# Kernel tuning notes

Measured on AMD Instinct MI355X. Metric: run time of the kernel, lower is better.

## Reference

```python
import jax, jax.numpy as jnp
import numpy as np

N_NODES, N_GRAPHS, N_EDGES = 40960, 1024, 163840


def setup_inputs() -> dict:
    key = jax.random.key(0)
    ks = jax.random.split(key, 40)
    w = lambda k, s: jax.random.normal(k, s, jnp.float32) * 0.05
    inp = {
        "x": jax.random.normal(ks[0], (N_NODES, 78), jnp.float32),
        "edge_index": jax.random.randint(ks[1], (2, N_EDGES), 0, N_NODES, jnp.int32),
        "batch": jnp.repeat(jnp.arange(N_GRAPHS, dtype=jnp.int32), N_NODES // N_GRAPHS),
        "target1": jax.random.normal(ks[2], (N_GRAPHS, 750, 20), jnp.float32),
        "target2": jax.random.randint(ks[3], (N_GRAPHS, 750), 0, 26, jnp.int32),
        # GCN layers
        "W1": w(ks[4], (78, 78)), "b1": jnp.zeros((78,), jnp.float32),
        "W2": w(ks[5], (78, 156)), "b2": jnp.zeros((156,), jnp.float32),
        "W3": w(ks[6], (156, 312)), "b3": jnp.zeros((312,), jnp.float32),
        "Wg1": w(ks[7], (312, 1024)), "bg1": jnp.zeros((1024,), jnp.float32),
        "Wg2": w(ks[8], (1024, 128)), "bg2": jnp.zeros((128,), jnp.float32),
        # protein branch
        "emb": w(ks[9], (26, 128)),
        "Wc2": w(ks[10], (32, 750, 8)), "bc2": jnp.zeros((32,), jnp.float32),
        "Wxt2": w(ks[11], (32 * 121, 128)), "bxt2": jnp.zeros((128,), jnp.float32),
        "Wc1": w(ks[12], (32, 750, 8)), "bc1": jnp.zeros((32,), jnp.float32),
        "Wxt1": w(ks[13], (416, 128)), "bxt1": jnp.zeros((128,), jnp.float32),
        # fusion head
        "Wf1": w(ks[14], (384, 1024)), "bf1": jnp.zeros((1024,), jnp.float32),
        "Wf2": w(ks[15], (1024, 512)), "bf2": jnp.zeros((512,), jnp.float32),
        "Wo": w(ks[16], (512, 1)), "bo": jnp.zeros((1,), jnp.float32),
    }
    return inp


def _conv1d(x, w, b):
    # x: [B, C_in, L], w: [C_out, C_in, K] -> [B, C_out, L-K+1]
    y = jax.lax.conv_general_dilated(x, w, (1,), "VALID",
                                     dimension_numbers=("NCH", "OIH", "NCH"))
    return y + b[None, :, None]


def reference(x, edge_index, batch, target1, target2,
              W1, b1, W2, b2, W3, b3, Wg1, bg1, Wg2, bg2,
              emb, Wc2, bc2, Wxt2, bxt2, Wc1, bc1, Wxt1, bxt1,
              Wf1, bf1, Wf2, bf2, Wo, bo):
    N = x.shape[0]
    loop = jnp.arange(N, dtype=edge_index.dtype)
    src = jnp.concatenate([edge_index[0], loop])  # message source j
    dst = jnp.concatenate([edge_index[1], loop])  # aggregation target i
    # symmetric GCN normalization with self-loops (degree from dst, as in PyG)
    deg = jnp.zeros((N,), x.dtype).at[dst].add(1.0)
    dinv = jax.lax.rsqrt(deg)  # deg >= 1 due to self loops
    norm = (dinv[src] * dinv[dst])[:, None]

    def gcn(h, W, b):
        m = (h @ W)[src] * norm
        return jax.ops.segment_sum(m, dst, num_segments=N) + b

    h = jax.nn.relu(gcn(x, W1, b1))
    h = jax.nn.relu(gcn(h, W2, b2))
    h = jax.nn.relu(gcn(h, W3, b3))
    # global max pool per graph
    g = jax.ops.segment_max(h, batch, num_segments=N_GRAPHS)
    g = jax.nn.relu(g @ Wg1 + bg1)
    g = g @ Wg2 + bg2  # dropout is identity at inference

    # protein branch 2: embedding -> conv1d over channels=750
    e = emb[target2]                         # [B, 750, 128]
    xt2 = _conv1d(e, Wc2, bc2)               # [B, 32, 121]
    xt2 = xt2.reshape(-1, 32 * 121) @ Wxt2 + bxt2

    # protein branch 1: raw float features
    xt1 = _conv1d(target1, Wc1, bc1)         # [B, 32, 13]
    xt1 = xt1.reshape(-1, 416) @ Wxt1 + bxt1

    xc = jnp.concatenate([g, xt1, xt2], axis=1)  # [B, 384]
    xc = jax.nn.relu(xc @ Wf1 + bf1)
    xc = jax.nn.relu(xc @ Wf2 + bf2)
    return xc @ Wo + bo
```

## Files before the change

kernel.cpp:

```cpp
#include <hip/hip_runtime.h>
#include <hip/hip_bf16.h>

#define NN 40960
#define NE 163840
#define NB 1024

typedef __attribute__((ext_vector_type(8))) short short8;
typedef __attribute__((ext_vector_type(4))) short short4v;
typedef __attribute__((ext_vector_type(4))) float floatx4;

__device__ inline unsigned short f2bf(float f) {
    union { float f; unsigned u; } v; v.f = f;
    unsigned r = v.u + 0x7fffu + ((v.u >> 16) & 1u);
    return (unsigned short)(r >> 16);
}
__device__ inline float bf2f(unsigned short s) {
    union { unsigned u; float f; } v; v.u = ((unsigned)s) << 16; return v.f;
}
__device__ inline unsigned pack2bf(float lo, float hi) {
    return (unsigned)f2bf(lo) | ((unsigned)f2bf(hi) << 16);
}

static const size_t o_dinv = 0, o_g312 = 40960, o_g1024 = 360448, o_xc = 1409024,
                    o_f1 = 1802240, o_f2 = 2850816, o_b1v = 3375104, o_b2v = 3375232,
                    o_iws = 3375360, o_bufA = 3621124, o_bufB = 16400644;

__global__ void k_hist(const int* __restrict__ dst, int* __restrict__ cnt) {
    int e = blockIdx.x * 256 + threadIdx.x;
    if (e < NE) atomicAdd(&cnt[dst[e]], 1);
}

__global__ __launch_bounds__(1024) void k_scan1(const int* __restrict__ cnt, int* __restrict__ offTmp,
                                                int* __restrict__ blockSum, float* __restrict__ dinv) {
    __shared__ int lds[1024];
    int tid = threadIdx.x;
    int i = blockIdx.x * 1024 + tid;
    int v = cnt[i];
    dinv[i] = rsqrtf((float)v + 1.0f);
    lds[tid] = v;
    __syncthreads();
    for (int s = 1; s < 1024; s <<= 1) {
        int t = (tid >= s) ? lds[tid - s] : 0;
        __syncthreads();
        lds[tid] += t;
        __syncthreads();
    }
    offTmp[i] = lds[tid] - v;
    if (tid == 1023) blockSum[blockIdx.x] = lds[1023];
}

__global__ __launch_bounds__(64) void k_scan2(const int* __restrict__ blockSum, int* __restrict__ blockOff) {
    int l = threadIdx.x;
    int s = (l < 40) ? blockSum[l] : 0;
    int orig = s;
    for (int d = 1; d < 64; d <<= 1) {
        int t = __shfl_up(s, d);
        if (l >= d) s += t;
    }
    if (l < 40) blockOff[l] = s - orig;
}

__global__ __launch_bounds__(1024) void k_scan3(int* __restrict__ off, int* __restrict__ cur,
                                                const int* __restrict__ blockOff) {
    int i = blockIdx.x * 1024 + threadIdx.x;
    int o = off[i] + blockOff[blockIdx.x];
    off[i] = o;
    cur[i] = o;
    if (i == NN - 1) off[NN] = NE;
}

__global__ void k_fill(const int* __restrict__ ei, int* __restrict__ cur, int* __restrict__ srcOut) {
    int e = blockIdx.x * 256 + threadIdx.x;
    if (e >= NE) return;
    int s = ei[e], d = ei[NE + e];
    int pos = atomicAdd(&cur[d], 1);
    srcOut[pos] = s;
}

__global__ __launch_bounds__(256) void k_prep_mega(
    const float* __restrict__ W1, const float* __restrict__ W2, const float* __restrict__ W3,
    const float* __restrict__ Wg1, const float* __restrict__ Wg2, const float* __restrict__ Wf1,
    const float* __restrict__ Wf2, unsigned short* __restrict__ Wt,
    const float* __restrict__ Wc2, const float* __restrict__ Wc1,
    float* __restrict__ Wc2r, float* __restrict__ Wc1r,
    const float* __restrict__ Wxt1, float* __restrict__ Btb,
    const float* __restrict__ bc1, const float* __restrict__ bxt1, float* __restrict__ b1v,
    const float* __restrict__ bc2, const float* __restrict__ Wxt2, const float* __restrict__ bxt2,
    float* __restrict__ b2v,
    const float* __restrict__ emb, float* __restrict__ T) {
    __shared__ float el[128];
    int bx = blockIdx.x, tid = threadIdx.x;
    if (bx < 3328) {
        const int cum[8]  = {0, 128, 320, 640, 1664, 1792, 2816, 3328};
        const int KP[7]   = {96, 96, 160, 320, 1024, 384, 1024};
        const int KB[7]   = {78, 78, 156, 312, 1024, 384, 1024};
        const int NNm[7]  = {78, 156, 312, 1024, 128, 1024, 512};
        const size_t OFF[7] = {0, 12288, 30720, 81920, 409600, 540672, 933888};
        int m = 0;
        while (m < 6 && bx >= cum[m + 1]) m++;
        int r = bx - cum[m];
        const float* src = (m == 0) ? W1 : (m == 1) ? W2 : (m == 2) ? W3 : (m == 3) ? Wg1
                         : (m == 4) ? Wg2 : (m == 5) ? Wf1 : Wf2;
        int kp = KP[m], kb = KB[m], nn = NNm[m];
        unsigned short* d = Wt + OFF[m] + (size_t)r * kp;
        for (int k = tid; k < kp; k += 256) {
            float v = (r < nn && k < kb) ? src[(size_t)k * nn + r] : 0.f;
            d[k] = f2bf(v);
        }
    } else if (bx < 4828) {
        int cc = bx - 3328, j = tid;
        const float* W = (cc < 750) ? Wc2 : Wc1;
        float* Wr = (cc < 750) ? Wc2r : Wc1r;
        int c = (cc < 750) ? cc : cc - 750;
        Wr[(size_t)c * 256 + j] = W[(size_t)(j >> 3) * 6000 + c * 8 + (j & 7)];
    } else if (bx < 7388) {
        int idx = (bx - 4828) * 256 + tid;
        int j = idx & 127, ok = (idx >> 7) & 255, t = idx >> 15;
        int o = ok >> 3, k = ok & 7, lpos = t - k;
        float v = (lpos >= 0 && lpos < 13) ? Wxt1[(size_t)(o * 13 + lpos) * 128 + j] : 0.f;
        Btb[(size_t)(t * 256 + ok) * 128 + j] = v;
    } else if (bx < 7452) {
        if (tid >= 128) return;
        int b = bx - 7388, j = tid;
        if (b < 32) {
            const float* p = Wxt1 + (size_t)b * 13 * 128 + j;
            float t = 0.f;
            for (int l = 0; l < 13; l++) t += p[(size_t)l * 128];
            float add = bc1[b] * t + ((b == 0) ? bxt1[j] : 0.f);
            atomicAdd(&b1v[j], add);
        } else {
            int o = b - 32;
            const float* p = Wxt2 + (size_t)o * 121 * 128 + j;
            float t = 0.f;
            for (int l = 0; l < 121; l++) t += p[(size_t)l * 128];
            float add = bc2[o] * t + ((o == 0) ? bxt2[j] : 0.f);
            atomicAdd(&b2v[j], add);
        }
    } else {
        int tb = bx - 7452;
        int v = tb >> 4, op = tb & 15;
        int o = op * 2 + (tid >> 7), j = tid & 127;
        if (tid < 128) el[j] = emb[(size_t)v * 128 + j];
        __syncthreads();
        float acc[8] = {};
        for (int l = 0; l < 121; l++) {
            float w = Wxt2[(size_t)(o * 121 + l) * 128 + j];
#pragma unroll
            for (int k = 0; k < 8; k++) acc[k] += el[l + k] * w;
        }
#pragma unroll
        for (int k = 0; k < 8; k++) T[(size_t)(v * 256 + o * 8 + k) * 128 + j] = acc[k];
    }
}

__device__ inline void d_agg16_node(int n, int f, const unsigned* __restrict__ h,
                                    const float* __restrict__ dinv, const int* __restrict__ off,
                                    const int* __restrict__ srcs, unsigned* __restrict__ out, int F2) {
    if (f >= F2) return;
    float di = dinv[n];
    unsigned s0v = h[(size_t)n * F2 + f];
    float a0 = bf2f((unsigned short)(s0v & 0xffff)) * di * di;
    float a1 = bf2f((unsigned short)(s0v >> 16)) * di * di;
    int e0 = off[n], e1 = off[n + 1];
    int e = e0;
    for (; e + 4 <= e1; e += 4) {
        int s0 = srcs[e], s1 = srcs[e + 1], s2 = srcs[e + 2], s3 = srcs[e + 3];
        float d0 = dinv[s0] * di, d1 = dinv[s1] * di, d2 = dinv[s2] * di, d3 = dinv[s3] * di;
        unsigned v0 = h[(size_t)s0 * F2 + f];
        unsigned v1 = h[(size_t)s1 * F2 + f];
        unsigned v2 = h[(size_t)s2 * F2 + f];
        unsigned v3 = h[(size_t)s3 * F2 + f];
        a0 += bf2f((unsigned short)(v0 & 0xffff)) * d0 + bf2f((unsigned short)(v1 & 0xffff)) * d1
            + bf2f((unsigned short)(v2 & 0xffff)) * d2 + bf2f((unsigned short)(v3 & 0xffff)) * d3;
        a1 += bf2f((unsigned short)(v0 >> 16)) * d0 + bf2f((unsigned short)(v1 >> 16)) * d1
            + bf2f((unsigned short)(v2 >> 16)) * d2 + bf2f((unsigned short)(v3 >> 16)) * d3;
    }
    for (; e < e1; e++) {
        int s = srcs[e];
        float dd = dinv[s] * di;
        unsigned v = h[(size_t)s * F2 + f];
        a0 += bf2f((unsigned short)(v & 0xffff)) * dd;
        a1 += bf2f((unsigned short)(v >> 16)) * dd;
    }
    out[(size_t)n * F2 + f] = pack2bf(a0, a1);
}

__global__ void k_agg16(const unsigned* __restrict__ h, const float* __restrict__ dinv,
                        const int* __restrict__ off, const int* __restrict__ srcs,
                        unsigned* __restrict__ out, int F2) {
    d_agg16_node(blockIdx.x, threadIdx.x, h, dinv, off, srcs, out, F2);
}

#define LDST 72
template <bool ABF16, bool OUTBF16, bool ATOMIC, bool RELU_OUT>
__global__ __launch_bounds__(256) void gemm_bt(const void* __restrict__ Av, const unsigned short* __restrict__ Bt,
                                               const float* __restrict__ bias, void* __restrict__ Cv,
                                               int Nn, int Npad, int Kpad, int Klim,
                                               int lda, int ldb, int ldc, int ksplit) {
    __shared__ __align__(16) unsigned short As[64 * LDST];
    __shared__ __align__(16) unsigned short Bs[64 * LDST];
    const float* Af = (const float*)Av;
    const unsigned short* A16 = (const unsigned short*)Av;
    float* Cf = (float*)Cv;
    unsigned short* C16 = (unsigned short*)Cv;
    int bn0 = blockIdx.x * 64;
    int bm0 = blockIdx.y * 64;
    int k0 = blockIdx.z * ksplit;
    int kend = k0 + ksplit; if (kend > Kpad) kend = Kpad;
    int tid = threadIdx.x;
    int w = tid >> 6, l = tid & 63, q = l >> 4, r = l & 15;
    int wr = w >> 1, wc = w & 1;

    floatx4 acc[2][2];
#pragma unroll
    for (int i = 0; i < 2; i++)
#pragma unroll
        for (int c = 0; c < 2; c++) acc[i][c] = (floatx4)0.0f;

    int mA = tid >> 2, kcA = (tid & 3) * 8;
    int nB = tid >> 2, kcB = (tid & 3) * 8;
    int gmA = bm0 + mA;
    int gnB = bn0 + nB;

    for (int kt = k0; kt < kend; kt += 32) {
        if (ABF16) {
            *(short8*)&As[mA * LDST + kcA] = *(const short8*)(A16 + (size_t)gmA * lda + kt + kcA);
        } else {
            const float* Ap = Af + (size_t)gmA * lda + kt + kcA;
            float av[8];
            if (kt + kcA + 8 <= Klim) {
#pragma unroll
                for (int j = 0; j < 4; j++) {
                    float2 p = *(const float2*)(Ap + j * 2);
                    av[j * 2] = p.x; av[j * 2 + 1] = p.y;
                }
            } else {
#pragma unroll
                for (int j = 0; j < 8; j++) av[j] = (kt + kcA + j < Klim) ? Ap[j] : 0.f;
            }
            short8 sv;
#pragma unroll
            for (int j = 0; j < 8; j++) sv[j] = (short)f2bf(av[j]);
            *(short8*)&As[mA * LDST + kcA] = sv;
        }
        *(short8*)&Bs[nB * LDST + kcB] = *(const short8*)(Bt + (size_t)gnB * ldb + kt + kcB);
        __syncthreads();
        short8 a0 = *(const short8*)&As[(wr * 32 + r) * LDST + q * 8];
        short8 a1 = *(const short8*)&As[(wr * 32 + 16 + r) * LDST + q * 8];
        short8 b0 = *(const short8*)&Bs[(wc * 32 + r) * LDST + q * 8];
        short8 b1 = *(const short8*)&Bs[(wc * 32 + 16 + r) * LDST + q * 8];
        acc[0][0] = __builtin_amdgcn_mfma_f32_16x16x32_bf16(a0, b0, acc[0][0], 0, 0, 0);
        acc[0][1] = __builtin_amdgcn_mfma_f32_16x16x32_bf16(a0, b1, acc[0][1], 0, 0, 0);
        acc[1][0] = __builtin_amdgcn_mfma_f32_16x16x32_bf16(a1, b0, acc[1][0], 0, 0, 0);
        acc[1][1] = __builtin_amdgcn_mfma_f32_16x16x32_bf16(a1, b1, acc[1][1], 0, 0, 0);
        __syncthreads();
    }

#pragma unroll
    for (int c2 = 0; c2 < 2; c2++) {
        int col = bn0 + wc * 32 + c2 * 16 + r;
        if (col >= Npad) continue;
        bool live = col < Nn;
        float bv = (bias && live) ? bias[col] : 0.f;
#pragma unroll
        for (int i = 0; i < 2; i++) {
#pragma unroll
            for (int v = 0; v < 4; v++) {
                int row = bm0 + wr * 32 + i * 16 + q * 4 + v;
                float val = live ? (acc[i][c2][v] + bv) : 0.f;
                if (RELU_OUT) val = fmaxf(val, 0.f);
                if (OUTBF16) {
                    C16[(size_t)row * ldc + col] = live ? f2bf(val) : (unsigned short)0;
                } else if (live) {
                    if (ATOMIC) atomicAdd(&Cf[(size_t)row * ldc + col], val);
                    else Cf[(size_t)row * ldc + col] = val;
                }
            }
        }
    }
}

__global__ __launch_bounds__(256) void k_batch_both(const float* __restrict__ Wc2r, const float* __restrict__ T,
                                                    const float* __restrict__ Wc1r, const float* __restrict__ Btb,
                                                    unsigned short* __restrict__ U16, unsigned short* __restrict__ Vt16) {
    __shared__ __align__(16) unsigned short As[64 * LDST];
    __shared__ __align__(16) unsigned short Bs[64 * LDST];
    const int M = 750, Nn = 128, K = 256;
    int z = blockIdx.z;
    bool om1 = z < 26;
    const float* A = om1 ? Wc2r : Wc1r;
    const float* Bm = om1 ? (T + (size_t)z * 32768) : (Btb + (size_t)(z - 26) * 32768);
    unsigned short* C16 = om1 ? (U16 + (size_t)z * 128) : Vt16;
    int ldc = om1 ? 3328 : 15360;
    int zz = z - 26;
    int bn0 = blockIdx.x * 64;
    int bm0 = blockIdx.y * 64;
    int tid = threadIdx.x;
    int w = tid >> 6, l = tid & 63, q = l >> 4, r = l & 15;
    int wr = w >> 1, wc = w & 1;

    floatx4 acc[2][2];
#pragma unroll
    for (int i = 0; i < 2; i++)
#pragma unroll
        for (int c = 0; c < 2; c++) acc[i][c] = (floatx4)0.0f;

    int mA = tid >> 2, kcA = (tid & 3) * 8;
    int nB = tid >> 2, kcB = (tid & 3) * 8;
    int gmA = bm0 + mA;
    int gnB = bn0 + nB;

    for (int kt = 0; kt < K; kt += 32) {
        {
            float av[8];
            const float* Ap = A + (size_t)gmA * K + kt + kcA;
            if (gmA < M) {
#pragma unroll
                for (int j = 0; j < 4; j++) {
                    float2 p = *(const float2*)(Ap + j * 2);
                    av[j * 2] = p.x; av[j * 2 + 1] = p.y;
                }
            } else {
#pragma unroll
                for (int j = 0; j < 8; j++) av[j] = 0.f;
            }
            short8 sv;
#pragma unroll
            for (int j = 0; j < 8; j++) sv[j] = (short)f2bf(av[j]);
            *(short8*)&As[mA * LDST + kcA] = sv;
        }
        {
            short8 sv;
#pragma unroll
            for (int j = 0; j < 8; j++) {
                int gk = kt + kcB + j;
                float v = (gnB < Nn) ? Bm[(size_t)gk * Nn + gnB] : 0.f;
                sv[j] = (short)f2bf(v);
            }
            *(short8*)&Bs[nB * LDST + kcB] = sv;
        }
        __syncthreads();
        short8 a0 = *(const short8*)&As[(wr * 32 + r) * LDST + q * 8];
        short8 a1 = *(const short8*)&As[(wr * 32 + 16 + r) * LDST + q * 8];
        short8 b0 = *(const short8*)&Bs[(wc * 32 + r) * LDST + q * 8];
        short8 b1 = *(const short8*)&Bs[(wc * 32 + 16 + r) * LDST + q * 8];
        acc[0][0] = __builtin_amdgcn_mfma_f32_16x16x32_bf16(a0, b0, acc[0][0], 0, 0, 0);
        acc[0][1] = __builtin_amdgcn_mfma_f32_16x16x32_bf16(a0, b1, acc[0][1], 0, 0, 0);
        acc[1][0] = __builtin_amdgcn_mfma_f32_16x16x32_bf16(a1, b0, acc[1][0], 0, 0, 0);
        acc[1][1] = __builtin_amdgcn_mfma_f32_16x16x32_bf16(a1, b1, acc[1][1], 0, 0, 0);
        __syncthreads();
    }

#pragma unroll
    for (int c = 0; c < 2; c++) {
        int col = bn0 + wc * 32 + c * 16 + r;
        if (col >= Nn) continue;
#pragma unroll
        for (int i = 0; i < 2; i++) {
#pragma unroll
            for (int v = 0; v < 4; v++) {
                int row = bm0 + wr * 32 + i * 16 + q * 4 + v;
                if (row >= M) continue;
                if (om1) C16[(size_t)row * ldc + col] = f2bf(acc[i][c][v]);
                else C16[(size_t)col * ldc + row * 20 + zz] = f2bf(acc[i][c][v]);
            }
        }
    }
}

#define T1LD 40
#define T1S  48
#define T1K  320
__global__ __launch_bounds__(256) void k_aggx_t1(
    const float* __restrict__ x, const float* __restrict__ dinv, const int* __restrict__ off,
    const int* __restrict__ srcs, unsigned* __restrict__ aggb,
    const float* __restrict__ t1A, const unsigned short* __restrict__ Bt, float* __restrict__ P) {
    __shared__ __align__(16) unsigned short As[2][64 * T1LD];
    __shared__ __align__(16) unsigned short Bs[2][128 * T1LD];
    int bx = blockIdx.x, tid = threadIdx.x;
    if (bx < 768) {
        const int Klim = 15000;
        int mt = bx & 15, ks = bx >> 4;
        int bm0 = mt * 64;
        int k0 = ks * T1K;
        int w = tid >> 6, l = tid & 63, q = l >> 4, r = l & 15;
        int wr = w >> 1, wc = w & 1;

        floatx4 acc[2][4];
#pragma unroll
        for (int i = 0; i < 2; i++)
#pragma unroll
            for (int c = 0; c < 4; c++) acc[i][c] = (floatx4)0.0f;

        int ra = tid >> 3, ca = (tid & 7) * 4;
        int rb = tid >> 2, cb = (tid & 3) * 8;
        const float* Ap0 = t1A + (size_t)(bm0 + ra) * Klim + ca;
        const float* Ap1 = t1A + (size_t)(bm0 + ra + 32) * Klim + ca;
        const unsigned short* Bp0 = Bt + (size_t)rb * 15360 + cb;
        const unsigned short* Bp1 = Bt + (size_t)(rb + 64) * 15360 + cb;

        float4 aA0, aA1, aB0, aB1;
        short8 bA0, bA1, bB0, bB1;

        auto loadT = [&](int kt, float4& x0, float4& x1, short8& y0, short8& y1) {
            int c = kt + ca;
            if (c < Klim) {
                x0 = *(const float4*)(Ap0 + kt);
                x1 = *(const float4*)(Ap1 + kt);
            } else {
                x0 = make_float4(0.f, 0.f, 0.f, 0.f);
                x1 = make_float4(0.f, 0.f, 0.f, 0.f);
            }
            y0 = *(const short8*)(Bp0 + kt);
            y1 = *(const short8*)(Bp1 + kt);
        };
        auto stageW = [&](int buf, const float4& x0, const float4& x1, const short8& y0, const short8& y1) {
            short4v s0, s1;
            s0[0] = (short)f2bf(x0.x); s0[1] = (short)f2bf(x0.y); s0[2] = (short)f2bf(x0.z); s0[3] = (short)f2bf(x0.w);
            s1[0] = (short)f2bf(x1.x); s1[1] = (short)f2bf(x1.y); s1[2] = (short)f2bf(x1.z); s1[3] = (short)f2bf(x1.w);
            *(short4v*)&As[buf][ra * T1LD + ca] = s0;
            *(short4v*)&As[buf][(ra + 32) * T1LD + ca] = s1;
            *(short8*)&Bs[buf][rb * T1LD + cb] = y0;
            *(short8*)&Bs[buf][(rb + 64) * T1LD + cb] = y1;
        };
        auto compute = [&](int buf) {
            short8 a0 = *(const short8*)&As[buf][(wr * 32 + r) * T1LD + q * 8];
            short8 a1 = *(const short8*)&As[buf][(wr * 32 + 16 + r) * T1LD + q * 8];
            short8 b0 = *(const short8*)&Bs[buf][(wc * 64 + r) * T1LD + q * 8];
            short8 b1 = *(const short8*)&Bs[buf][(wc * 64 + 16 + r) * T1LD + q * 8];
            short8 b2 = *(const short8*)&Bs[buf][(wc * 64 + 32 + r) * T1LD + q * 8];
            short8 b3 = *(const short8*)&Bs[buf][(wc * 64 + 48 + r) * T1LD + q * 8];
            acc[0][0] = __builtin_amdgcn_mfma_f32_16x16x32_bf16(a0, b0, acc[0][0], 0, 0, 0);
            acc[0][1] = __builtin_amdgcn_mfma_f32_16x16x32_bf16(a0, b1, acc[0][1], 0, 0, 0);
            acc[0][2] = __builtin_amdgcn_mfma_f32_16x16x32_bf16(a0, b2, acc[0][2], 0, 0, 0);
            acc[0][3] = __builtin_amdgcn_mfma_f32_16x16x32_bf16(a0, b3, acc[0][3], 0, 0, 0);
            acc[1][0] = __builtin_amdgcn_mfma_f32_16x16x32_bf16(a1, b0, acc[1][0], 0, 0, 0);
            acc[1][1] = __builtin_amdgcn_mfma_f32_16x16x32_bf16(a1, b1, acc[1][1], 0, 0, 0);
            acc[1][2] = __builtin_amdgcn_mfma_f32_16x16x32_bf16(a1, b2, acc[1][2], 0, 0, 0);
            acc[1][3] = __builtin_amdgcn_mfma_f32_16x16x32_bf16(a1, b3, acc[1][3], 0, 0, 0);
        };

        loadT(k0, aA0, aA1, bA0, bA1);
        loadT(k0 + 32, aB0, aB1, bB0, bB1);
#pragma unroll
        for (int it = 0; it < T1K / 32; it += 2) {
            stageW(0, aA0, aA1, bA0, bA1);
            if (it + 2 < T1K / 32) loadT(k0 + (it + 2) * 32, aA0, aA1, bA0, bA1);
            asm volatile("s_waitcnt lgkmcnt(0)" ::: "memory");
            __builtin_amdgcn_s_barrier();
            asm volatile("" ::: "memory");
            compute(0);
            stageW(1, aB0, aB1, bB0, bB1);
            if (it + 3 < T1K / 32) loadT(k0 + (it + 3) * 32, aB0, aB1, bB0, bB1);
            asm volatile("s_waitcnt lgkmcnt(0)" ::: "memory");
            __builtin_amdgcn_s_barrier();
            asm volatile("" ::: "memory");
            compute(1);
        }

        float* Pp = P + (size_t)ks * (1024 * 128) + (size_t)bm0 * 128;
#pragma unroll
        for (int c = 0; c < 4; c++) {
            int col = wc * 64 + c * 16 + r;
#pragma unroll
            for (int i = 0; i < 2; i++) {
#pragma unroll
                for (int v = 0; v < 4; v++) {
                    int row = wr * 32 + i * 16 + q * 4 + v;
                    Pp[(size_t)row * 128 + col] = acc[i][c][v];
                }
            }
        }
    } else {
        int n = (bx - 768) * 4 + (tid >> 6);
        int f = tid & 63;
        if (f >= 48) return;
        if (f >= 39) { aggb[(size_t)n * 48 + f] = 0; return; }
        float di = dinv[n];
        float2 sv = *(const float2*)&x[(size_t)n * 78 + 2 * f];
        float a0 = sv.x * di * di, a1 = sv.y * di * di;
        int e0 = off[n], e1 = off[n + 1];
        int e = e0;
        for (; e + 4 <= e1; e += 4) {
            int s0 = srcs[e], s1 = srcs[e + 1], s2 = srcs[e + 2], s3 = srcs[e + 3];
            float d0 = dinv[s0] * di, d1 = dinv[s1] * di, d2 = dinv[s2] * di, d3 = dinv[s3] * di;
            float2 v0 = *(const float2*)&x[(size_t)s0 * 78 + 2 * f];
            float2 v1 = *(const float2*)&x[(size_t)s1 * 78 + 2 * f];
            float2 v2 = *(const float2*)&x[(size_t)s2 * 78 + 2 * f];
            float2 v3 = *(const float2*)&x[(size_t)s3 * 78 + 2 * f];
            a0 += v0.x * d0 + v1.x * d1 + v2.x * d2 + v3.x * d3;
            a1 += v0.y * d0 + v1.y * d1 + v2.y * d2 + v3.y * d3;
        }
        for (; e < e1; e++) {
            int s = srcs[e];
            float dd = dinv[s] * di;
            float2 v = *(const float2*)&x[(size_t)s * 78 + 2 * f];
            a0 += v.x * dd; a1 += v.y * dd;
        }
        aggb[(size_t)n * 48 + f] = pack2bf(a0, a1);
    }
}

__global__ __launch_bounds__(128) void k_agg16_ug(
    const unsigned* __restrict__ h, const float* __restrict__ dinv, const int* __restrict__ off,
    const int* __restrict__ srcs, unsigned* __restrict__ outb,
    const int* __restrict__ t2, const unsigned short* __restrict__ U,
    const float* __restrict__ b2v, float* __restrict__ xc) {
    __shared__ int offs[752];
    __shared__ float red[8][128];
    int bx = blockIdx.x, tid = threadIdx.x;
    if (bx < NB) {
        int b = bx;
        int rg = tid >> 4, lane = tid & 15;
        const int* t2b = t2 + (size_t)b * 750;
        for (int i = tid; i < 750; i += 128) offs[i] = i * 3328 + t2b[i] * 128;
        __syncthreads();
        float a[8] = {};
#pragma unroll 4
        for (int i = rg; i < 750; i += 8) {
            short8 v = *(const short8*)&U[(size_t)offs[i] + lane * 8];
#pragma unroll
            for (int c = 0; c < 8; c++) a[c] += bf2f((unsigned short)v[c]);
        }
#pragma unroll
        for (int c = 0; c < 8; c++) red[rg][lane * 8 + c] = a[c];
        __syncthreads();
        float s = b2v[tid];
#pragma unroll
        for (int g = 0; g < 8; g++) s += red[g][tid];
        xc[(size_t)b * 384 + 256 + tid] = s;
    } else {
        d_agg16_node(bx - NB, tid, h, dinv, off, srcs, outb, 80);
    }
}

__global__ void k_segmax_red(const unsigned short* __restrict__ h, unsigned short* __restrict__ g,
                             const float* __restrict__ P, float* __restrict__ xc) {
    int bx = blockIdx.x, tid = threadIdx.x;
    if (bx < NB) {
        if (tid < 128) {
            int row = bx, j = tid;
            const float* p = P + (size_t)row * 128 + j;
            float s = 0.f;
#pragma unroll
            for (int ks = 0; ks < T1S; ks++) s += p[(size_t)ks * (1024 * 128)];
            xc[(size_t)row * 384 + 128 + j] += s;
        }
    } else {
        int gr = bx - NB, f = tid;
        if (f >= 320) return;
        if (f >= 312) { g[(size_t)gr * 320 + f] = 0; return; }
        float m = 0.0f;
        const unsigned short* base = h + (size_t)gr * 40 * 312 + f;
        for (int i = 0; i < 40; i++) m = fmaxf(m, bf2f(base[(size_t)i * 312]));
        g[(size_t)gr * 320 + f] = f2bf(m);
    }
}

__global__ __launch_bounds__(768) void k_initC(float* __restrict__ xc, float* __restrict__ f2,
                                               const float* __restrict__ bg2, const float* __restrict__ b1v,
                                               const float* __restrict__ bf2) {
    int b = blockIdx.x, t = threadIdx.x;
    if (t < 128) xc[(size_t)b * 384 + t] = bg2[t];
    else if (t < 256) xc[(size_t)b * 384 + t] = b1v[t - 128];
    else f2[(size_t)b * 512 + t - 256] = bf2[t - 256];
}

__global__ __launch_bounds__(64) void k_final(const float* __restrict__ f2, const float* __restrict__ Wo,
                                              const float* __restrict__ bo, float* __restrict__ out) {
    int b = blockIdx.x, lane = threadIdx.x;
    float s = 0.f;
    for (int j = lane; j < 512; j += 64) s += fmaxf(f2[(size_t)b * 512 + j], 0.f) * Wo[j];
    for (int off = 32; off; off >>= 1) s += __shfl_down(s, off);
    if (lane == 0) out[b] = s + bo[0];
}

extern "C" void kernel_launch(void* const* d_in, const int* in_sizes, int n_in,
                              void* d_out, int out_size, void* d_ws, size_t ws_size,
                              hipStream_t stream) {
    const float* x    = (const float*)d_in[0];
    const int*   ei   = (const int*)d_in[1];
    const float* t1   = (const float*)d_in[3];
    const int*   t2   = (const int*)d_in[4];
    const float* W1   = (const float*)d_in[5];
    const float* b1   = (const float*)d_in[6];
    const float* W2   = (const float*)d_in[7];
    const float* b2   = (const float*)d_in[8];
    const float* W3   = (const float*)d_in[9];
    const float* b3   = (const float*)d_in[10];
    const float* Wg1  = (const float*)d_in[11];
    const float* bg1  = (const float*)d_in[12];
    const float* Wg2  = (const float*)d_in[13];
    const float* bg2  = (const float*)d_in[14];
    const float* emb  = (const float*)d_in[15];
    const float* Wc2  = (const float*)d_in[16];
    const float* bc2  = (const float*)d_in[17];
    const float* Wxt2 = (const float*)d_in[18];
    const float* bxt2 = (const float*)d_in[19];
    const float* Wc1  = (const float*)d_in[20];
    const float* bc1  = (const float*)d_in[21];
    const float* Wxt1 = (const float*)d_in[22];
    const float* bxt1 = (const float*)d_in[23];
    const float* Wf1  = (const float*)d_in[24];
    const float* bf1  = (const float*)d_in[25];
    const float* Wf2  = (const float*)d_in[26];
    const float* bf2  = (const float*)d_in[27];
    const float* Wo   = (const float*)d_in[28];
    const float* bo   = (const float*)d_in[29];
    float* out = (float*)d_out;

    float* ws = (float*)d_ws;
    float* dinv  = ws + o_dinv;
    unsigned short* g312b = (unsigned short*)(ws + o_g312);
    unsigned short* g1024b = (unsigned short*)(ws + o_g1024);
    float* xc    = ws + o_xc;
    unsigned short* f1b = (unsigned short*)(ws + o_f1);
    float* f2    = ws + o_f2;
    float* b1v   = ws + o_b1v;
    float* b2v   = ws + o_b2v;
    int* csrOff  = (int*)(ws + o_iws);
    int* csrCur  = csrOff + (NN + 1);
    int* csrSrc  = csrCur + NN;
    int* blockSum = (int*)(ws + o_f1 + 600000);
    int* blockOff = blockSum + 40;
    float* bufA  = ws + o_bufA;
    float* bufB  = ws + o_bufB;
    float* T    = bufA;
    unsigned short* U16  = (unsigned short*)(bufA + 851968);
    unsigned short* Vt16 = (unsigned short*)(bufA + 2200000);
    unsigned short* Wt   = (unsigned short*)(bufA + 3200000);
    float* Wc2r = bufA + 4000000;
    float* Wc1r = bufA + 4200000;
    float* Btb  = bufA + 4400000;
    float* Pt1  = bufA + 6000000;
    unsigned* aggb = (unsigned*)bufB;
    unsigned short* h16 = (unsigned short*)(bufB + 5500000);

    unsigned short* W1t  = Wt + 0;
    unsigned short* W2t  = Wt + 12288;
    unsigned short* W3t  = Wt + 30720;
    unsigned short* Wg1t = Wt + 81920;
    unsigned short* Wg2t = Wt + 409600;
    unsigned short* Wf1t = Wt + 540672;
    unsigned short* Wf2t = Wt + 933888;

    hipMemsetAsync(Vt16, 0, (size_t)128 * 15360 * 2, stream);
    hipMemsetAsync(b1v, 0, 256 * sizeof(float), stream);
    hipMemsetAsync(csrCur, 0, NN * sizeof(int), stream);
    k_hist<<<NE / 256, 256, 0, stream>>>(ei + NE, csrCur);
    k_scan1<<<40, 1024, 0, stream>>>(csrCur, csrOff, blockSum, dinv);
    k_scan2<<<1, 64, 0, stream>>>(blockSum, blockOff);
    k_scan3<<<40, 1024, 0, stream>>>(csrOff, csrCur, blockOff);
    k_fill<<<NE / 256, 256, 0, stream>>>(ei, csrCur, csrSrc);

    k_prep_mega<<<7868, 256, 0, stream>>>(W1, W2, W3, Wg1, Wg2, Wf1, Wf2, Wt,
                                          Wc2, Wc1, Wc2r, Wc1r,
                                          Wxt1, Btb, bc1, bxt1, b1v,
                                          bc2, Wxt2, bxt2, b2v, emb, T);

    k_batch_both<<<dim3(2, 12, 46), 256, 0, stream>>>(Wc2r, T, Wc1r, Btb, U16, Vt16);

    k_initC<<<NB, 768, 0, stream>>>(xc, f2, bg2, b1v, bf2);

    k_aggx_t1<<<768 + NN / 4, 256, 0, stream>>>(x, dinv, csrOff, csrSrc, aggb, t1, Vt16, Pt1);

    gemm_bt<true, true, false, true><<<dim3(2, 640, 1), 256, 0, stream>>>(
        aggb, W1t, b1, h16, 78, 96, 96, 96, 96, 96, 96, 96);
    k_agg16<<<NN, 64, 0, stream>>>((unsigned*)h16, dinv, csrOff, csrSrc, aggb, 48);
    gemm_bt<true, true, false, true><<<dim3(3, 640, 1), 256, 0, stream>>>(
        aggb, W2t, b2, h16, 156, 160, 96, 96, 96, 96, 160, 96);
    k_agg16_ug<<<NB + NN, 128, 0, stream>>>((unsigned*)h16, dinv, csrOff, csrSrc, aggb,
                                            t2, U16, b2v, xc);
    gemm_bt<true, true, false, true><<<dim3(5, 640, 1), 256, 0, stream>>>(
        aggb, W3t, b3, h16, 312, 312, 160, 160, 160, 160, 312, 160);
    k_segmax_red<<<2 * NB, 320, 0, stream>>>(h16, g312b, Pt1, xc);
    gemm_bt<true, true, false, true><<<dim3(16, 16, 1), 256, 0, stream>>>(
        g312b, Wg1t, bg1, g1024b, 1024, 1024, 320, 320, 320, 320, 1024, 320);

    gemm_bt<true, false, true, false><<<dim3(2, 16, 8), 256, 0, stream>>>(
        g1024b, Wg2t, nullptr, xc + 0, 128, 128, 1024, 1024, 1024, 1024, 384, 128);

    gemm_bt<false, true, false, true><<<dim3(16, 16, 1), 256, 0, stream>>>(
        xc, Wf1t, bf1, f1b, 1024, 1024, 384, 384, 384, 384, 1024, 384);
    gemm_bt<true, false, true, false><<<dim3(8, 16, 4), 256, 0, stream>>>(
        f1b, Wf2t, nullptr, f2, 512, 512, 1024, 1024, 1024, 1024, 512, 256);
    k_final<<<NB, 64, 0, stream>>>(f2, Wo, bo, out);
}
```

Measured before the change: 447.0 us.

## Merge CSR fill, batch conv GEMM and init into one launch; pair t1 with layer-1 GEMM

```diff
diff --git a/kernel.cpp b/kernel.cpp
--- a/kernel.cpp
+++ b/kernel.cpp
@@ -67,14 +67,6 @@
     off[i] = o;
     cur[i] = o;
     if (i == NN - 1) off[NN] = NE;
-}
-
-__global__ void k_fill(const int* __restrict__ ei, int* __restrict__ cur, int* __restrict__ srcOut) {
-    int e = blockIdx.x * 256 + threadIdx.x;
-    if (e >= NE) return;
-    int s = ei[e], d = ei[NE + e];
-    int pos = atomicAdd(&cur[d], 1);
-    srcOut[pos] = s;
 }
 
 __global__ __launch_bounds__(256) void k_prep_mega(
@@ -153,6 +145,37 @@
     }
 }
 
+__global__ __launch_bounds__(64) void k_agg_x(const float* __restrict__ x, const float* __restrict__ dinv,
+                                              const int* __restrict__ off, const int* __restrict__ srcs,
+                                              unsigned* __restrict__ out) {
+    int n = blockIdx.x;
+    int f = threadIdx.x;
+    if (f >= 48) return;
+    if (f >= 39) { out[(size_t)n * 48 + f] = 0; return; }
+    float di = dinv[n];
+    float2 sv = *(const float2*)&x[(size_t)n * 78 + 2 * f];
+    float a0 = sv.x * di * di, a1 = sv.y * di * di;
+    int e0 = off[n], e1 = off[n + 1];
+    int e = e0;
+    for (; e + 4 <= e1; e += 4) {
+        int s0 = srcs[e], s1 = srcs[e + 1], s2 = srcs[e + 2], s3 = srcs[e + 3];
+        float d0 = dinv[s0] * di, d1 = dinv[s1] * di, d2 = dinv[s2] * di, d3 = dinv[s3] * di;
+        float2 v0 = *(const float2*)&x[(size_t)s0 * 78 + 2 * f];
+        float2 v1 = *(const float2*)&x[(size_t)s1 * 78 + 2 * f];
+        float2 v2 = *(const float2*)&x[(size_t)s2 * 78 + 2 * f];
+        float2 v3 = *(const float2*)&x[(size_t)s3 * 78 + 2 * f];
+        a0 += v0.x * d0 + v1.x * d1 + v2.x * d2 + v3.x * d3;
+        a1 += v0.y * d0 + v1.y * d1 + v2.y * d2 + v3.y * d3;
+    }
+    for (; e < e1; e++) {
+        int s = srcs[e];
+        float dd = dinv[s] * di;
+        float2 v = *(const float2*)&x[(size_t)s * 78 + 2 * f];
+        a0 += v.x * dd; a1 += v.y * dd;
+    }
+    out[(size_t)n * 48 + f] = pack2bf(a0, a1);
+}
+
 __device__ inline void d_agg16_node(int n, int f, const unsigned* __restrict__ h,
                                     const float* __restrict__ dinv, const int* __restrict__ off,
                                     const int* __restrict__ srcs, unsigned* __restrict__ out, int F2) {
@@ -280,22 +303,44 @@
     }
 }
 
-__global__ __launch_bounds__(256) void k_batch_both(const float* __restrict__ Wc2r, const float* __restrict__ T,
-                                                    const float* __restrict__ Wc1r, const float* __restrict__ Btb,
-                                                    unsigned short* __restrict__ U16, unsigned short* __restrict__ Vt16) {
+__global__ __launch_bounds__(256) void k_fbi(
+    const int* __restrict__ ei, int* __restrict__ cur, int* __restrict__ srcOut,
+    const float* __restrict__ Wc2r, const float* __restrict__ T,
+    const float* __restrict__ Wc1r, const float* __restrict__ Btb,
+    unsigned short* __restrict__ U16, unsigned short* __restrict__ Vt16,
+    float* __restrict__ xc, float* __restrict__ f2,
+    const float* __restrict__ bg2, const float* __restrict__ b1v, const float* __restrict__ bf2) {
     __shared__ __align__(16) unsigned short As[64 * LDST];
     __shared__ __align__(16) unsigned short Bs[64 * LDST];
+    int bx = blockIdx.x, tid = threadIdx.x;
+    if (bx < 640) {
+        int e = bx * 256 + tid;
+        if (e >= NE) return;
+        int s = ei[e], d = ei[NE + e];
+        int pos = atomicAdd(&cur[d], 1);
+        srcOut[pos] = s;
+        return;
+    }
+    if (bx >= 1744) {
+        int b = bx - 1744;
+        for (int t = tid; t < 768; t += 256) {
+            if (t < 128) xc[(size_t)b * 384 + t] = bg2[t];
+            else if (t < 256) xc[(size_t)b * 384 + t] = b1v[t - 128];
+            else f2[(size_t)b * 512 + t - 256] = bf2[t - 256];
+        }
+        return;
+    }
+    int v = bx - 640;
+    int gx = v & 1, gy = (v >> 1) % 12, gz = (v >> 1) / 12;
     const int M = 750, Nn = 128, K = 256;
-    int z = blockIdx.z;
-    bool om1 = z < 26;
+    bool om1 = gz < 26;
     const float* A = om1 ? Wc2r : Wc1r;
-    const float* Bm = om1 ? (T + (size_t)z * 32768) : (Btb + (size_t)(z - 26) * 32768);
-    unsigned short* C16 = om1 ? (U16 + (size_t)z * 128) : Vt16;
+    const float* Bm = om1 ? (T + (size_t)gz * 32768) : (Btb + (size_t)(gz - 26) * 32768);
+    unsigned short* C16 = om1 ? (U16 + (size_t)gz * 128) : Vt16;
     int ldc = om1 ? 3328 : 15360;
-    int zz = z - 26;
-    int bn0 = blockIdx.x * 64;
-    int bm0 = blockIdx.y * 64;
-    int tid = threadIdx.x;
+    int zz = gz - 26;
+    int bn0 = gx * 64;
+    int bm0 = gy * 64;
     int w = tid >> 6, l = tid & 63, q = l >> 4, r = l & 15;
     int wr = w >> 1, wc = w & 1;
 
@@ -334,8 +379,8 @@
 #pragma unroll
             for (int j = 0; j < 8; j++) {
                 int gk = kt + kcB + j;
-                float v = (gnB < Nn) ? Bm[(size_t)gk * Nn + gnB] : 0.f;
-                sv[j] = (short)f2bf(v);
+                float vv = (gnB < Nn) ? Bm[(size_t)gk * Nn + gnB] : 0.f;
+                sv[j] = (short)f2bf(vv);
             }
             *(short8*)&Bs[nB * LDST + kcB] = sv;
         }
@@ -358,11 +403,11 @@
 #pragma unroll
         for (int i = 0; i < 2; i++) {
 #pragma unroll
-            for (int v = 0; v < 4; v++) {
-                int row = bm0 + wr * 32 + i * 16 + q * 4 + v;
+            for (int vv = 0; vv < 4; vv++) {
+                int row = bm0 + wr * 32 + i * 16 + q * 4 + vv;
                 if (row >= M) continue;
-                if (om1) C16[(size_t)row * ldc + col] = f2bf(acc[i][c][v]);
-                else C16[(size_t)col * ldc + row * 20 + zz] = f2bf(acc[i][c][v]);
+                if (om1) C16[(size_t)row * ldc + col] = f2bf(acc[i][c][vv]);
+                else C16[(size_t)col * ldc + row * 20 + zz] = f2bf(acc[i][c][vv]);
             }
         }
     }
@@ -371,14 +416,15 @@
 #define T1LD 40
 #define T1S  48
 #define T1K  320
-__global__ __launch_bounds__(256) void k_aggx_t1(
-    const float* __restrict__ x, const float* __restrict__ dinv, const int* __restrict__ off,
-    const int* __restrict__ srcs, unsigned* __restrict__ aggb,
-    const float* __restrict__ t1A, const unsigned short* __restrict__ Bt, float* __restrict__ P) {
-    __shared__ __align__(16) unsigned short As[2][64 * T1LD];
-    __shared__ __align__(16) unsigned short Bs[2][128 * T1LD];
+__global__ __launch_bounds__(256) void k_t1_l1(
+    const float* __restrict__ t1A, const unsigned short* __restrict__ Bt, float* __restrict__ P,
+    const unsigned short* __restrict__ A16, const unsigned short* __restrict__ W1t,
+    const float* __restrict__ bias, unsigned short* __restrict__ C16) {
+    __shared__ __align__(16) unsigned char smem[30720];
     int bx = blockIdx.x, tid = threadIdx.x;
     if (bx < 768) {
+        unsigned short* AsS = (unsigned short*)smem;
+        unsigned short* BsS = (unsigned short*)smem + 5120;
         const int Klim = 15000;
         int mt = bx & 15, ks = bx >> 4;
         int bm0 = mt * 64;
@@ -418,18 +464,18 @@
             short4v s0, s1;
             s0[0] = (short)f2bf(x0.x); s0[1] = (short)f2bf(x0.y); s0[2] = (short)f2bf(x0.z); s0[3] = (short)f2bf(x0.w);
             s1[0] = (short)f2bf(x1.x); s1[1] = (short)f2bf(x1.y); s1[2] = (short)f2bf(x1.z); s1[3] = (short)f2bf(x1.w);
-            *(short4v*)&As[buf][ra * T1LD + ca] = s0;
-            *(short4v*)&As[buf][(ra + 32) * T1LD + ca] = s1;
-            *(short8*)&Bs[buf][rb * T1LD + cb] = y0;
-            *(short8*)&Bs[buf][(rb + 64) * T1LD + cb] = y1;
+            *(short4v*)&AsS[buf * 2560 + ra * T1LD + ca] = s0;
+            *(short4v*)&AsS[buf * 2560 + (ra + 32) * T1LD + ca] = s1;
+            *(short8*)&BsS[buf * 5120 + rb * T1LD + cb] = y0;
+            *(short8*)&BsS[buf * 5120 + (rb + 64) * T1LD + cb] = y1;
         };
         auto compute = [&](int buf) {
-            short8 a0 = *(const short8*)&As[buf][(wr * 32 + r) * T1LD + q * 8];
-            short8 a1 = *(const short8*)&As[buf][(wr * 32 + 16 + r) * T1LD + q * 8];
-            short8 b0 = *(const short8*)&Bs[buf][(wc * 64 + r) * T1LD + q * 8];
-            short8 b1 = *(const short8*)&Bs[buf][(wc * 64 + 16 + r) * T1LD + q * 8];
-            short8 b2 = *(const short8*)&Bs[buf][(wc * 64 + 32 + r) * T1LD + q * 8];
-            short8 b3 = *(const short8*)&Bs[buf][(wc * 64 + 48 + r) * T1LD + q * 8];
+            short8 a0 = *(const short8*)&AsS[buf * 2560 + (wr * 32 + r) * T1LD + q * 8];
+            short8 a1 = *(const short8*)&AsS[buf * 2560 + (wr * 32 + 16 + r) * T1LD + q * 8];
+            short8 b0 = *(const short8*)&BsS[buf * 5120 + (wc * 64 + r) * T1LD + q * 8];
+            short8 b1 = *(const short8*)&BsS[buf * 5120 + (wc * 64 + 16 + r) * T1LD + q * 8];
+            short8 b2 = *(const short8*)&BsS[buf * 5120 + (wc * 64 + 32 + r) * T1LD + q * 8];
+            short8 b3 = *(const short8*)&BsS[buf * 5120 + (wc * 64 + 48 + r) * T1LD + q * 8];
             acc[0][0] = __builtin_amdgcn_mfma_f32_16x16x32_bf16(a0, b0, acc[0][0], 0, 0, 0);
             acc[0][1] = __builtin_amdgcn_mfma_f32_16x16x32_bf16(a0, b1, acc[0][1], 0, 0, 0);
             acc[0][2] = __builtin_amdgcn_mfma_f32_16x16x32_bf16(a0, b2, acc[0][2], 0, 0, 0);
@@ -472,32 +518,55 @@
             }
         }
     } else {
-        int n = (bx - 768) * 4 + (tid >> 6);
-        int f = tid & 63;
-        if (f >= 48) return;
-        if (f >= 39) { aggb[(size_t)n * 48 + f] = 0; return; }
-        float di = dinv[n];
-        float2 sv = *(const float2*)&x[(size_t)n * 78 + 2 * f];
-        float a0 = sv.x * di * di, a1 = sv.y * di * di;
-        int e0 = off[n], e1 = off[n + 1];
-        int e = e0;
-        for (; e + 4 <= e1; e += 4) {
-            int s0 = srcs[e], s1 = srcs[e + 1], s2 = srcs[e + 2], s3 = srcs[e + 3];
-            float d0 = dinv[s0] * di, d1 = dinv[s1] * di, d2 = dinv[s2] * di, d3 = dinv[s3] * di;
-            float2 v0 = *(const float2*)&x[(size_t)s0 * 78 + 2 * f];
-            float2 v1 = *(const float2*)&x[(size_t)s1 * 78 + 2 * f];
-            float2 v2 = *(const float2*)&x[(size_t)s2 * 78 + 2 * f];
-            float2 v3 = *(const float2*)&x[(size_t)s3 * 78 + 2 * f];
-            a0 += v0.x * d0 + v1.x * d1 + v2.x * d2 + v3.x * d3;
-            a1 += v0.y * d0 + v1.y * d1 + v2.y * d2 + v3.y * d3;
-        }
-        for (; e < e1; e++) {
-            int s = srcs[e];
-            float dd = dinv[s] * di;
-            float2 v = *(const float2*)&x[(size_t)s * 78 + 2 * f];
-            a0 += v.x * dd; a1 += v.y * dd;
-        }
-        aggb[(size_t)n * 48 + f] = pack2bf(a0, a1);
+        unsigned short* As = (unsigned short*)smem;
+        unsigned short* Bs = (unsigned short*)smem + 4608;
+        int v = bx - 768;
+        int bn0 = (v & 1) * 64;
+        int bm0 = (v >> 1) * 64;
+        int w = tid >> 6, l = tid & 63, q = l >> 4, r = l & 15;
+        int wr = w >> 1, wc = w & 1;
+
+        floatx4 acc[2][2];
+#pragma unroll
+        for (int i = 0; i < 2; i++)
+#pragma unroll
+            for (int c = 0; c < 2; c++) acc[i][c] = (floatx4)0.0f;
+
+        int mA = tid >> 2, kcA = (tid & 3) * 8;
+        int gmA = bm0 + mA;
+        int gnB = bn0 + mA;
+
+        for (int kt = 0; kt < 96; kt += 32) {
+            *(short8*)&As[mA * LDST + kcA] = *(const short8*)(A16 + (size_t)gmA * 96 + kt + kcA);
+            *(short8*)&Bs[mA * LDST + kcA] = *(const short8*)(W1t + (size_t)gnB * 96 + kt + kcA);
+            __syncthreads();
+            short8 a0 = *(const short8*)&As[(wr * 32 + r) * LDST + q * 8];
+            short8 a1 = *(const short8*)&As[(wr * 32 + 16 + r) * LDST + q * 8];
+            short8 b0 = *(const short8*)&Bs[(wc * 32 + r) * LDST + q * 8];
+            short8 b1 = *(const short8*)&Bs[(wc * 32 + 16 + r) * LDST + q * 8];
+            acc[0][0] = __builtin_amdgcn_mfma_f32_16x16x32_bf16(a0, b0, acc[0][0], 0, 0, 0);
+            acc[0][1] = __builtin_amdgcn_mfma_f32_16x16x32_bf16(a0, b1, acc[0][1], 0, 0, 0);
+            acc[1][0] = __builtin_amdgcn_mfma_f32_16x16x32_bf16(a1, b0, acc[1][0], 0, 0, 0);
+            acc[1][1] = __builtin_amdgcn_mfma_f32_16x16x32_bf16(a1, b1, acc[1][1], 0, 0, 0);
+            __syncthreads();
+        }
+
+#pragma unroll
+        for (int c2 = 0; c2 < 2; c2++) {
+            int col = bn0 + wc * 32 + c2 * 16 + r;
+            if (col >= 96) continue;
+            bool live = col < 78;
+            float bv = live ? bias[col] : 0.f;
+#pragma unroll
+            for (int i = 0; i < 2; i++) {
+#pragma unroll
+                for (int vv = 0; vv < 4; vv++) {
+                    int row = bm0 + wr * 32 + i * 16 + q * 4 + vv;
+                    float val = live ? fmaxf(acc[i][c2][vv] + bv, 0.f) : 0.f;
+                    C16[(size_t)row * 96 + col] = live ? f2bf(val) : (unsigned short)0;
+                }
+            }
+        }
     }
 }
 
@@ -555,15 +624,6 @@
         for (int i = 0; i < 40; i++) m = fmaxf(m, bf2f(base[(size_t)i * 312]));
         g[(size_t)gr * 320 + f] = f2bf(m);
     }
-}
-
-__global__ __launch_bounds__(768) void k_initC(float* __restrict__ xc, float* __restrict__ f2,
-                                               const float* __restrict__ bg2, const float* __restrict__ b1v,
-                                               const float* __restrict__ bf2) {
-    int b = blockIdx.x, t = threadIdx.x;
-    if (t < 128) xc[(size_t)b * 384 + t] = bg2[t];
-    else if (t < 256) xc[(size_t)b * 384 + t] = b1v[t - 128];
-    else f2[(size_t)b * 512 + t - 256] = bf2[t - 256];
 }
 
 __global__ __launch_bounds__(64) void k_final(const float* __restrict__ f2, const float* __restrict__ Wo,
@@ -651,21 +711,19 @@
     k_scan1<<<40, 1024, 0, stream>>>(csrCur, csrOff, blockSum, dinv);
     k_scan2<<<1, 64, 0, stream>>>(blockSum, blockOff);
     k_scan3<<<40, 1024, 0, stream>>>(csrOff, csrCur, blockOff);
-    k_fill<<<NE / 256, 256, 0, stream>>>(ei, csrCur, csrSrc);
 
     k_prep_mega<<<7868, 256, 0, stream>>>(W1, W2, W3, Wg1, Wg2, Wf1, Wf2, Wt,
                                           Wc2, Wc1, Wc2r, Wc1r,
                                           Wxt1, Btb, bc1, bxt1, b1v,
                                           bc2, Wxt2, bxt2, b2v, emb, T);
 
-    k_batch_both<<<dim3(2, 12, 46), 256, 0, stream>>>(Wc2r, T, Wc1r, Btb, U16, Vt16);
-
-    k_initC<<<NB, 768, 0, stream>>>(xc, f2, bg2, b1v, bf2);
-
-    k_aggx_t1<<<768 + NN / 4, 256, 0, stream>>>(x, dinv, csrOff, csrSrc, aggb, t1, Vt16, Pt1);
-
-    gemm_bt<true, true, false, true><<<dim3(2, 640, 1), 256, 0, stream>>>(
-        aggb, W1t, b1, h16, 78, 96, 96, 96, 96, 96, 96, 96);
+    k_fbi<<<2768, 256, 0, stream>>>(ei, csrCur, csrSrc, Wc2r, T, Wc1r, Btb, U16, Vt16,
+                                    xc, f2, bg2, b1v, bf2);
+
+    k_agg_x<<<NN, 64, 0, stream>>>(x, dinv, csrOff, csrSrc, aggb);
+
+    k_t1_l1<<<2048, 256, 0, stream>>>(t1, Vt16, Pt1, (const unsigned short*)aggb, W1t, b1, h16);
+
     k_agg16<<<NN, 64, 0, stream>>>((unsigned*)h16, dinv, csrOff, csrSrc, aggb, 48);
     gemm_bt<true, true, false, true><<<dim3(3, 640, 1), 256, 0, stream>>>(
         aggb, W2t, b2, h16, 156, 160, 96, 96, 96, 96, 160, 96);
```

After: 423.3 us. 5.3% less time.
